# Performance work log

Measured on AMD Instinct MI355X. Metric: run time of the kernel, lower is better.

The kernel has to match this reference:

```python
import jax, jax.numpy as jnp
import numpy as np

B, S, D, DFF, H, V, L = 2, 1024, 1024, 4096, 16, 32000, 8
DH = D // H
EPS = 1e-5

def _pe():
    pos = np.arange(S, dtype=np.float32)[:, None]
    div = np.exp(np.arange(0, D, 2, dtype=np.float32) * (-np.log(10000.0) / D))
    pe = np.zeros((S, D), dtype=np.float32)
    pe[:, 0::2] = np.sin(pos * div)
    pe[:, 1::2] = np.cos(pos * div)
    return jnp.asarray(pe)

PE = _pe()

def _ln(h, g, b):
    m = jnp.mean(h, axis=-1, keepdims=True)
    v = jnp.mean((h - m) ** 2, axis=-1, keepdims=True)
    return (h - m) * jax.lax.rsqrt(v + EPS) * g + b

def setup_inputs():
    key = jax.random.key(0)
    k = jax.random.split(key, 16)
    sc = 0.02
    return {
        'x': jax.random.randint(k[0], (B, S), 0, V),
        'mask': jnp.tril(jnp.ones((1, 1, S, S), dtype=bool)),
        'emb': jax.random.normal(k[1], (V, D)) * sc,
        'Wq': jax.random.normal(k[2], (L, D, D)) * sc,
        'Wk': jax.random.normal(k[3], (L, D, D)) * sc,
        'Wv': jax.random.normal(k[4], (L, D, D)) * sc,
        'Wo': jax.random.normal(k[5], (L, D, D)) * sc,
        'ln1_g': jnp.ones((L, D)), 'ln1_b': jnp.zeros((L, D)),
        'ln2_g': jnp.ones((L, D)), 'ln2_b': jnp.zeros((L, D)),
        'W1': jax.random.normal(k[6], (L, D, DFF)) * sc,
        'b1': jnp.zeros((L, DFF)),
        'W2': jax.random.normal(k[7], (L, DFF, D)) * sc,
        'b2': jnp.zeros((L, D)),
        'lnf_g': jnp.ones((D,)), 'lnf_b': jnp.zeros((D,)),
        'projW': jax.random.normal(k[8], (D, V)) * sc,
        'projb': jnp.zeros((V,)),
    }

def reference(x, mask, emb, Wq, Wk, Wv, Wo, ln1_g, ln1_b, ln2_g, ln2_b,
              W1, b1, W2, b2, lnf_g, lnf_b, projW, projb):
    # embedding * sqrt(D) + positional encoding
    h = emb[x] * jnp.sqrt(jnp.float32(D)) + PE[None, :, :]
    scale = 1.0 / jnp.sqrt(jnp.float32(DH))
    for i in range(L):
        # --- self-attention sublayer (pre-LN residual) ---
        a_in = _ln(h, ln1_g[i], ln1_b[i])
        q = (a_in @ Wq[i]).reshape(B, S, H, DH)
        kk = (a_in @ Wk[i]).reshape(B, S, H, DH)
        v = (a_in @ Wv[i]).reshape(B, S, H, DH)
        scores = jnp.einsum('bqhd,bkhd->bhqk', q, kk) * scale
        scores = jnp.where(mask, scores, -1e9)
        attn = jax.nn.softmax(scores, axis=-1)
        o = jnp.einsum('bhqk,bkhd->bqhd', attn, v).reshape(B, S, D)
        h = h + o @ Wo[i]
        # --- feed-forward sublayer ---
        f_in = _ln(h, ln2_g[i], ln2_b[i])
        h = h + (jax.nn.relu(f_in @ W1[i] + b1[i]) @ W2[i] + b2[i])
    h = _ln(h, lnf_g, lnf_b)
    return h @ projW + projb
```

## Files before the change

### kernel.cpp

```cpp
#include <hip/hip_runtime.h>

typedef __bf16 bf16;
typedef __bf16 bf16x4 __attribute__((ext_vector_type(4)));
typedef __bf16 bf16x8 __attribute__((ext_vector_type(8)));
typedef float f32x4 __attribute__((ext_vector_type(4)));
typedef short short4v __attribute__((ext_vector_type(4)));

__device__ __forceinline__ short f2bs(float x) {
  bf16 hv = (bf16)x;
  return __builtin_bit_cast(short, hv);
}

__device__ __forceinline__ void gl_lds16(const void* g, void* l) {
  __builtin_amdgcn_global_load_lds(
      (const __attribute__((address_space(1))) unsigned int*)g,
      (__attribute__((address_space(3))) unsigned int*)l, 16, 0, 0);
}

__global__ __launch_bounds__(256) void wt_k(const float* __restrict__ in,
    bf16* __restrict__ out, int K, int N, long in_ls, long out_ls)
{
  __shared__ float t[64][33];
  const int z = blockIdx.z;
  const float* ip = in + (size_t)z * in_ls;
  bf16* op = out + (size_t)z * out_ls;
  const int n0 = blockIdx.x * 32, k0 = blockIdx.y * 64;
  const int tid = threadIdx.x;
  const int kr = tid >> 3, nc = (tid & 7) * 4;
#pragma unroll
  for (int hh = 0; hh < 2; ++hh) {
    float4 v = *(const float4*)(ip + (size_t)(k0 + kr + hh * 32) * N + n0 + nc);
    t[kr + hh * 32][nc]     = v.x;
    t[kr + hh * 32][nc + 1] = v.y;
    t[kr + hh * 32][nc + 2] = v.z;
    t[kr + hh * 32][nc + 3] = v.w;
  }
  __syncthreads();
  const int nr = tid >> 3, kc = (tid & 7) * 8;
  bf16x8 o;
#pragma unroll
  for (int j = 0; j < 8; ++j) o[j] = (bf16)t[kc + j][nr];
  *(bf16x8*)(op + (size_t)(n0 + nr) * K + k0 + kc) = o;
}

__global__ __launch_bounds__(256) void embed_k(const int* __restrict__ x,
    const float* __restrict__ emb, float* __restrict__ h)
{
  const int m = blockIdx.x, t = threadIdx.x;
  const int s = m & 1023;
  const int tok = x[m];
  const int d0 = t * 4;
  float4 e = *(const float4*)(emb + (size_t)tok * 1024 + d0);
  const float* ep = &e.x;
  float r[4];
#pragma unroll
  for (int j = 0; j < 4; ++j) {
    int d = d0 + j;
    float freq = expf((float)(d & ~1) * (-9.2103403719761836f / 1024.f));
    float ang = (float)s * freq;
    float pe = (d & 1) ? cosf(ang) : sinf(ang);
    r[j] = ep[j] * 32.f + pe;
  }
  *(float4*)(h + (size_t)m * 1024 + d0) = make_float4(r[0], r[1], r[2], r[3]);
}

__global__ __launch_bounds__(256) void ln_k(const float* __restrict__ h,
    const float* __restrict__ g, const float* __restrict__ b,
    bf16* __restrict__ out)
{
  const int row = blockIdx.x, t = threadIdx.x;
  const float* hr = h + (size_t)row * 1024;
  float4 x = *(const float4*)(hr + t * 4);
  float s  = x.x + x.y + x.z + x.w;
  float ss = x.x * x.x + x.y * x.y + x.z * x.z + x.w * x.w;
#pragma unroll
  for (int off = 32; off >= 1; off >>= 1) {
    s  += __shfl_down(s, off);
    ss += __shfl_down(ss, off);
  }
  __shared__ float sb[4], ssb[4];
  if ((t & 63) == 0) { sb[t >> 6] = s; ssb[t >> 6] = ss; }
  __syncthreads();
  s  = sb[0] + sb[1] + sb[2] + sb[3];
  ss = ssb[0] + ssb[1] + ssb[2] + ssb[3];
  const float mean = s * (1.f / 1024.f);
  const float var  = ss * (1.f / 1024.f) - mean * mean;
  const float rstd = rsqrtf(var + 1e-5f);
  const float* xp = &x.x;
#pragma unroll
  for (int j = 0; j < 4; ++j) {
    int d = t * 4 + j;
    out[(size_t)row * 1024 + d] = (bf16)((xp[j] - mean) * rstd * g[d] + b[d]);
  }
}

template<int MODE, int NSPLIT>
__global__ __launch_bounds__(256) void gemm3_k(
    const bf16* __restrict__ A, const bf16* __restrict__ Bt,
    const float* __restrict__ bias, void* __restrict__ Cout,
    float* __restrict__ Hacc, bf16* __restrict__ Vt,
    int M, int N, int K)
{
  __shared__ __align__(16) bf16 As[2][128 * 64];
  __shared__ __align__(16) bf16 Bs[2][128 * 64];

  const int nwg = gridDim.x;
  const int orig = blockIdx.x;
  const int q8 = nwg >> 3, r8 = nwg & 7;
  const int xcd = orig & 7, loc = orig >> 3;
  const int wg = (xcd < r8 ? xcd * (q8 + 1) : r8 * (q8 + 1) + (xcd - r8) * q8) + loc;
  const int nrowt = M >> 7;
  const int ntiles = nrowt * (N >> 7);
  const int split = (NSPLIT > 1) ? (wg / ntiles) : 0;
  const int tile  = (NSPLIT > 1) ? (wg % ntiles) : wg;
  const int rowt = tile & (nrowt - 1);
  const int colt = tile / nrowt;
  const int m0 = rowt * 128;
  const int n0 = colt * 128;
  const int Ks = K / NSPLIT;
  const int k_begin = split * Ks;
  const int nt = Ks >> 6;

  const int tid = threadIdx.x;
  const int lane = tid & 63;
  const int wbase = tid & ~63;
  const int wid = tid >> 6;
  const int wm = wid >> 1, wn = wid & 1;
  const int qr = lane & 15, grp = lane >> 4;

  f32x4 acc[4][4];
#pragma unroll
  for (int i = 0; i < 4; ++i)
#pragma unroll
    for (int j = 0; j < 4; ++j) acc[i][j] = (f32x4){0.f, 0.f, 0.f, 0.f};

  auto stage = [&](int bufi, int kt) {
#pragma unroll
    for (int it = 0; it < 4; ++it) {
      const int idx = it * 256 + tid;
      const int row = idx >> 3, c = idx & 7;
      const int bo = (c * 16) ^ ((row & 7) << 4);
      gl_lds16((const char*)(A + (size_t)(m0 + row) * K + kt) + bo,
               (char*)&As[bufi][0] + (size_t)(it * 256 + wbase) * 16);
    }
#pragma unroll
    for (int it = 0; it < 4; ++it) {
      const int idx = it * 256 + tid;
      const int row = idx >> 3, c = idx & 7;
      const int bo = (c * 16) ^ ((row & 7) << 4);
      gl_lds16((const char*)(Bt + (size_t)(n0 + row) * K + kt) + bo,
               (char*)&Bs[bufi][0] + (size_t)(it * 256 + wbase) * 16);
    }
  };

  stage(0, k_begin);
  asm volatile("s_waitcnt vmcnt(0)" ::: "memory");
  __builtin_amdgcn_s_barrier();

  for (int t = 0; t < nt; ++t) {
    const int cur = t & 1;
    if (t + 1 < nt) stage(cur ^ 1, k_begin + (t + 1) * 64);
#pragma unroll
    for (int ks = 0; ks < 2; ++ks) {
      bf16x8 af[4], bfr[4];
#pragma unroll
      for (int mi = 0; mi < 4; ++mi) {
        const int arow = wm * 64 + mi * 16 + qr;
        const int ab = arow * 128 + ((grp * 16 + ks * 64) ^ ((arow & 7) << 4));
        af[mi] = *(const bf16x8*)((const char*)&As[cur][0] + ab);
      }
#pragma unroll
      for (int ni = 0; ni < 4; ++ni) {
        const int brow = wn * 64 + ni * 16 + qr;
        const int bb = brow * 128 + ((grp * 16 + ks * 64) ^ ((brow & 7) << 4));
        bfr[ni] = *(const bf16x8*)((const char*)&Bs[cur][0] + bb);
      }
#pragma unroll
      for (int mi = 0; mi < 4; ++mi)
#pragma unroll
        for (int ni = 0; ni < 4; ++ni)
          acc[mi][ni] = __builtin_amdgcn_mfma_f32_16x16x32_bf16(
              af[mi], bfr[ni], acc[mi][ni], 0, 0, 0);
    }
    asm volatile("s_waitcnt vmcnt(0)" ::: "memory");
    __builtin_amdgcn_s_barrier();
  }

  const int sel = (MODE == 5) ? (n0 >> 10) : 0;
#pragma unroll
  for (int ni = 0; ni < 4; ++ni) {
    const int coln = wn * 64 + ni * 16 + qr;
    const int colg = n0 + coln;
    float bv = 0.f;
    if (MODE == 1 || MODE == 4) bv = bias[colg];
    if (MODE == 3 && split == 0) bv = bias[colg];
#pragma unroll
    for (int mi = 0; mi < 4; ++mi) {
      const int rowg0 = m0 + wm * 64 + mi * 16 + grp * 4;
      if (MODE == 5 && sel == 2) {
        const int b = rowg0 >> 10, s = rowg0 & 1023;
        bf16x4 pv;
#pragma unroll
        for (int r = 0; r < 4; ++r) pv[r] = (bf16)acc[mi][ni][r];
        *(bf16x4*)(Vt + (size_t)b * 1024 * 1024 + (size_t)(colg & 1023) * 1024 + s) = pv;
      } else {
#pragma unroll
        for (int r = 0; r < 4; ++r) {
          const int rowg = rowg0 + r;
          float v = acc[mi][ni][r];
          if (MODE == 1) {
            v += bv; v = v > 0.f ? v : 0.f;
            ((bf16*)Cout)[(size_t)rowg * N + colg] = (bf16)v;
          } else if (MODE == 2) {
            if (NSPLIT > 1) atomicAdd(&Hacc[(size_t)rowg * N + colg], v);
            else            Hacc[(size_t)rowg * N + colg] += v;
          } else if (MODE == 3) {
            if (NSPLIT > 1) atomicAdd(&Hacc[(size_t)rowg * N + colg], v + bv);
            else            Hacc[(size_t)rowg * N + colg] += v + bv;
          } else if (MODE == 4) {
            ((float*)Cout)[(size_t)rowg * N + colg] = v + bv;
          } else {
            bf16* cb = (bf16*)Cout + (size_t)sel * 2048 * 1024;
            cb[(size_t)rowg * 1024 + (colg & 1023)] = (bf16)v;
          }
        }
      }
    }
  }
}

__global__ __launch_bounds__(64) void attn_k(const bf16* __restrict__ qm,
    const bf16* __restrict__ km, const bf16* __restrict__ vt,
    bf16* __restrict__ om)
{
  const int lane = threadIdx.x;
  const int qr = lane & 15, g = lane >> 4;
  const int qt = blockIdx.x & 63;
  const int hh = (blockIdx.x >> 6) & 15;
  const int bb = blockIdx.x >> 10;
  const size_t rowb = (size_t)bb * 1024;
  const int hb = hh * 64;

  const bf16* qp = qm + (rowb + qt * 16 + qr) * 1024 + hb + g * 8;
  const bf16x8 qf0 = *(const bf16x8*)qp;
  const bf16x8 qf1 = *(const bf16x8*)(qp + 32);

  float m_run = -1e30f, l_run = 0.f;
  f32x4 oacc[4];
#pragma unroll
  for (int dt = 0; dt < 4; ++dt) oacc[dt] = (f32x4){0.f, 0.f, 0.f, 0.f};

  const int qglob = qt * 16 + qr;
  const bf16* vtb = vt + (size_t)bb * 1024 * 1024;

  for (int kvt = 0; kvt <= qt; ++kvt) {
    const bf16* kp = km + (rowb + kvt * 16 + qr) * 1024 + hb + g * 8;
    bf16x8 kf0 = *(const bf16x8*)kp;
    bf16x8 kf1 = *(const bf16x8*)(kp + 32);
    f32x4 st = (f32x4){0.f, 0.f, 0.f, 0.f};
    st = __builtin_amdgcn_mfma_f32_16x16x32_bf16(kf0, qf0, st, 0, 0, 0);
    st = __builtin_amdgcn_mfma_f32_16x16x32_bf16(kf1, qf1, st, 0, 0, 0);

    float sc[4];
#pragma unroll
    for (int r = 0; r < 4; ++r) {
      int kvg = kvt * 16 + g * 4 + r;
      sc[r] = (kvg <= qglob) ? st[r] * 0.125f : -1e30f;
    }
    float mloc = fmaxf(fmaxf(sc[0], sc[1]), fmaxf(sc[2], sc[3]));
    mloc = fmaxf(mloc, __shfl_xor(mloc, 16));
    mloc = fmaxf(mloc, __shfl_xor(mloc, 32));
    float m_new = fmaxf(m_run, mloc);
    float alpha = __expf(m_run - m_new);
    float p[4], ps = 0.f;
#pragma unroll
    for (int r = 0; r < 4; ++r) { p[r] = __expf(sc[r] - m_new); ps += p[r]; }
    ps += __shfl_xor(ps, 16);
    ps += __shfl_xor(ps, 32);
    l_run = l_run * alpha + ps;
    m_run = m_new;

    short4v pf;
#pragma unroll
    for (int r = 0; r < 4; ++r) pf[r] = f2bs(p[r]);
#pragma unroll
    for (int dt = 0; dt < 4; ++dt) oacc[dt] *= alpha;

#pragma unroll
    for (int dt = 0; dt < 4; ++dt) {
      short4v vf = __builtin_bit_cast(short4v,
          *(const bf16x4*)(vtb + (size_t)(hb + dt * 16 + qr) * 1024 + kvt * 16 + g * 4));
      oacc[dt] = __builtin_amdgcn_mfma_f32_16x16x16bf16_1k(vf, pf, oacc[dt], 0, 0, 0);
    }
  }

  const float inv = 1.f / l_run;
  bf16* op = om + (rowb + qt * 16 + qr) * 1024 + hb;
#pragma unroll
  for (int dt = 0; dt < 4; ++dt)
#pragma unroll
    for (int r = 0; r < 4; ++r)
      op[dt * 16 + g * 4 + r] = (bf16)(oacc[dt][r] * inv);
}

extern "C" void kernel_launch(void* const* d_in, const int* in_sizes, int n_in,
                              void* d_out, int out_size, void* d_ws, size_t ws_size,
                              hipStream_t stream)
{
  (void)in_sizes; (void)n_in; (void)out_size; (void)ws_size;
  const int*   x     = (const int*)d_in[0];
  const float* emb   = (const float*)d_in[2];
  const float* Wq    = (const float*)d_in[3];
  const float* Wk    = (const float*)d_in[4];
  const float* Wv    = (const float*)d_in[5];
  const float* Wo    = (const float*)d_in[6];
  const float* ln1g  = (const float*)d_in[7];
  const float* ln1b  = (const float*)d_in[8];
  const float* ln2g  = (const float*)d_in[9];
  const float* ln2b  = (const float*)d_in[10];
  const float* W1    = (const float*)d_in[11];
  const float* b1    = (const float*)d_in[12];
  const float* W2    = (const float*)d_in[13];
  const float* b2    = (const float*)d_in[14];
  const float* lnfg  = (const float*)d_in[15];
  const float* lnfb  = (const float*)d_in[16];
  const float* projW = (const float*)d_in[17];
  const float* projb = (const float*)d_in[18];

  char* ws = (char*)d_ws;
  const size_t MB = 1u << 20;
  float* h    = (float*)(ws + 0);
  bf16*  ain  = (bf16*)(ws + 8 * MB);
  bf16*  qb   = (bf16*)(ws + 12 * MB);
  bf16*  kb   = (bf16*)(ws + 16 * MB);
  bf16*  vtb  = (bf16*)(ws + 20 * MB);
  bf16*  ob   = (bf16*)(ws + 24 * MB);
  bf16*  mid  = (bf16*)(ws + 28 * MB);
  bf16*  Bqkv = (bf16*)(ws + 44 * MB);
  bf16*  Bo   = (bf16*)(ws + 92 * MB);
  bf16*  B1t  = (bf16*)(ws + 108 * MB);
  bf16*  B2t  = (bf16*)(ws + 172 * MB);
  bf16*  Bprj = (bf16*)(ws + 236 * MB);

  const long M1 = 1024 * 1024, M3 = 3 * M1, M4 = 4 * M1;

  wt_k<<<dim3(32, 16, 8),   256, 0, stream>>>(Wq, Bqkv,          1024, 1024, M1, M3);
  wt_k<<<dim3(32, 16, 8),   256, 0, stream>>>(Wk, Bqkv + M1,     1024, 1024, M1, M3);
  wt_k<<<dim3(32, 16, 8),   256, 0, stream>>>(Wv, Bqkv + 2 * M1, 1024, 1024, M1, M3);
  wt_k<<<dim3(32, 16, 8),   256, 0, stream>>>(Wo, Bo,            1024, 1024, M1, M1);
  wt_k<<<dim3(128, 16, 8),  256, 0, stream>>>(W1, B1t,           1024, 4096, M4, M4);
  wt_k<<<dim3(32, 64, 8),   256, 0, stream>>>(W2, B2t,           4096, 1024, M4, M4);
  wt_k<<<dim3(1000, 16, 1), 256, 0, stream>>>(projW, Bprj,       1024, 32000, 0, 0);

  embed_k<<<dim3(2048), 256, 0, stream>>>(x, emb, h);
  for (int i = 0; i < 8; ++i) {
    ln_k<<<dim3(2048), 256, 0, stream>>>(h, ln1g + i * 1024, ln1b + i * 1024, ain);
    gemm3_k<5,1><<<dim3(384), 256, 0, stream>>>(ain, Bqkv + i * M3, nullptr,
                                                qb, nullptr, vtb, 2048, 3072, 1024);
    attn_k<<<dim3(2048), 64, 0, stream>>>(qb, kb, vtb, ob);
    gemm3_k<2,2><<<dim3(256), 256, 0, stream>>>(ob, Bo + i * M1, nullptr,
                                                nullptr, h, nullptr, 2048, 1024, 1024);
    ln_k<<<dim3(2048), 256, 0, stream>>>(h, ln2g + i * 1024, ln2b + i * 1024, ain);
    gemm3_k<1,1><<<dim3(512), 256, 0, stream>>>(ain, B1t + i * M4, b1 + i * 4096,
                                                mid, nullptr, nullptr, 2048, 4096, 1024);
    gemm3_k<3,2><<<dim3(256), 256, 0, stream>>>(mid, B2t + i * M4, b2 + i * 1024,
                                                nullptr, h, nullptr, 2048, 1024, 4096);
  }
  ln_k<<<dim3(2048), 256, 0, stream>>>(h, lnfg, lnfb, ain);
  gemm3_k<4,1><<<dim3(4000), 256, 0, stream>>>(ain, Bprj, projb,
                                               d_out, nullptr, nullptr, 2048, 32000, 1024);
}
```

Baseline: 2.197 ms.

## Use 256x256-tile GEMM for vocab projection and unroll unmasked attention tiles

Adds a 512-thread GEMM kernel with 256x256 tiles, swizzled LDS double buffering and a staggered B prefetch, and uses it for the final 32000-wide output projection in place of the 128-tile generic GEMM. The goal is more operand reuse per loaded byte. The attention kernel now processes off-diagonal KV tiles two at a time without mask checks, and only the diagonal tile is masked, which cuts per-tile compare and shuffle overhead and gives more loads in flight. The larger tile uses much more LDS and registers, which may limit occupancy.

```diff
diff --git a/kernel.cpp b/kernel.cpp
--- a/kernel.cpp
+++ b/kernel.cpp
@@ -91,6 +91,111 @@
   for (int j = 0; j < 4; ++j) {
     int d = t * 4 + j;
     out[(size_t)row * 1024 + d] = (bf16)((xp[j] - mean) * rstd * g[d] + b[d]);
+  }
+}
+
+__global__ __launch_bounds__(512, 2) void gemm256_k(
+    const bf16* __restrict__ A, const bf16* __restrict__ Bt,
+    const float* __restrict__ bias, float* __restrict__ C,
+    int M, int N, int K)
+{
+  __shared__ __align__(16) bf16 As[2][256 * 64];
+  __shared__ __align__(16) bf16 Bs[2][256 * 64];
+
+  const int nwg = gridDim.x;
+  const int orig = blockIdx.x;
+  const int q8 = nwg >> 3, r8 = nwg & 7;
+  const int xcd = orig & 7, loc = orig >> 3;
+  const int wg = (xcd < r8 ? xcd * (q8 + 1) : r8 * (q8 + 1) + (xcd - r8) * q8) + loc;
+  const int nrowt = M >> 8;
+  const int rowt = wg & (nrowt - 1);
+  const int colt = wg / nrowt;
+  const int m0 = rowt * 256;
+  const int n0 = colt * 256;
+  const int nt = K >> 6;
+
+  const int tid = threadIdx.x;
+  const int lane = tid & 63;
+  const int wbase = tid & ~63;
+  const int wid = tid >> 6;
+  const int wm = wid >> 2, wn = wid & 3;
+  const int qr = lane & 15, grp = lane >> 4;
+
+  f32x4 acc[8][4];
+#pragma unroll
+  for (int i = 0; i < 8; ++i)
+#pragma unroll
+    for (int j = 0; j < 4; ++j) acc[i][j] = (f32x4){0.f, 0.f, 0.f, 0.f};
+
+  auto stageA = [&](int bufi, int kt) {
+#pragma unroll
+    for (int it = 0; it < 4; ++it) {
+      const int idx = it * 512 + tid;
+      const int row = idx >> 3, c = idx & 7;
+      const int bo = (c * 16) ^ ((row & 7) << 4);
+      gl_lds16((const char*)(A + (size_t)(m0 + row) * K + kt) + bo,
+               (char*)&As[bufi][0] + (size_t)(it * 512 + wbase) * 16);
+    }
+  };
+  auto stageB = [&](int bufi, int kt) {
+#pragma unroll
+    for (int it = 0; it < 4; ++it) {
+      const int idx = it * 512 + tid;
+      const int row = idx >> 3, c = idx & 7;
+      const int bo = (c * 16) ^ ((row & 7) << 4);
+      gl_lds16((const char*)(Bt + (size_t)(n0 + row) * K + kt) + bo,
+               (char*)&Bs[bufi][0] + (size_t)(it * 512 + wbase) * 16);
+    }
+  };
+
+  stageA(0, 0); stageB(0, 0);
+  asm volatile("s_waitcnt vmcnt(0)" ::: "memory");
+  __builtin_amdgcn_s_barrier();
+
+  for (int t = 0; t < nt; ++t) {
+    const int cur = t & 1;
+    const bool pfch = (t + 1 < nt);
+    if (pfch) stageA(cur ^ 1, (t + 1) * 64);
+#pragma unroll
+    for (int ks = 0; ks < 2; ++ks) {
+      bf16x8 af[8], bfr[4];
+#pragma unroll
+      for (int mi = 0; mi < 8; ++mi) {
+        const int arow = wm * 128 + mi * 16 + qr;
+        const int ab = arow * 128 + ((grp * 16 + ks * 64) ^ ((arow & 7) << 4));
+        af[mi] = *(const bf16x8*)((const char*)&As[cur][0] + ab);
+      }
+#pragma unroll
+      for (int ni = 0; ni < 4; ++ni) {
+        const int brow = wn * 64 + ni * 16 + qr;
+        const int bb = brow * 128 + ((grp * 16 + ks * 64) ^ ((brow & 7) << 4));
+        bfr[ni] = *(const bf16x8*)((const char*)&Bs[cur][0] + bb);
+      }
+      __builtin_amdgcn_s_setprio(1);
+#pragma unroll
+      for (int mi = 0; mi < 8; ++mi)
+#pragma unroll
+        for (int ni = 0; ni < 4; ++ni)
+          acc[mi][ni] = __builtin_amdgcn_mfma_f32_16x16x32_bf16(
+              af[mi], bfr[ni], acc[mi][ni], 0, 0, 0);
+      __builtin_amdgcn_s_setprio(0);
+      if (ks == 0 && pfch) stageB(cur ^ 1, (t + 1) * 64);
+    }
+    asm volatile("s_waitcnt vmcnt(0)" ::: "memory");
+    __builtin_amdgcn_s_barrier();
+  }
+
+#pragma unroll
+  for (int ni = 0; ni < 4; ++ni) {
+    const int colg = n0 + wn * 64 + ni * 16 + qr;
+    const float bv = bias[colg];
+#pragma unroll
+    for (int mi = 0; mi < 8; ++mi) {
+      const int rowg0 = m0 + wm * 128 + mi * 16 + grp * 4;
+#pragma unroll
+      for (int r = 0; r < 4; ++r)
+        C[(size_t)(rowg0 + r) * N + colg] = acc[mi][ni][r] + bv;
+    }
   }
 }
 
@@ -192,7 +297,7 @@
     const int coln = wn * 64 + ni * 16 + qr;
     const int colg = n0 + coln;
     float bv = 0.f;
-    if (MODE == 1 || MODE == 4) bv = bias[colg];
+    if (MODE == 1) bv = bias[colg];
     if (MODE == 3 && split == 0) bv = bias[colg];
 #pragma unroll
     for (int mi = 0; mi < 4; ++mi) {
@@ -217,9 +322,7 @@
           } else if (MODE == 3) {
             if (NSPLIT > 1) atomicAdd(&Hacc[(size_t)rowg * N + colg], v + bv);
             else            Hacc[(size_t)rowg * N + colg] += v + bv;
-          } else if (MODE == 4) {
-            ((float*)Cout)[(size_t)rowg * N + colg] = v + bv;
-          } else {
+          } else if (MODE == 5) {
             bf16* cb = (bf16*)Cout + (size_t)sel * 2048 * 1024;
             cb[(size_t)rowg * 1024 + (colg & 1023)] = (bf16)v;
           }
@@ -252,20 +355,24 @@
 
   const int qglob = qt * 16 + qr;
   const bf16* vtb = vt + (size_t)bb * 1024 * 1024;
-
-  for (int kvt = 0; kvt <= qt; ++kvt) {
-    const bf16* kp = km + (rowb + kvt * 16 + qr) * 1024 + hb + g * 8;
+  const bf16* kbase = km + rowb * 1024 + hb;
+
+  auto tile_step = [&](int kvt, bool masked) {
+    const bf16* kp = kbase + (size_t)kvt * 16 * 1024 + qr * 1024 + g * 8;
     bf16x8 kf0 = *(const bf16x8*)kp;
     bf16x8 kf1 = *(const bf16x8*)(kp + 32);
+    bf16x4 vf[4];
+#pragma unroll
+    for (int dt = 0; dt < 4; ++dt)
+      vf[dt] = *(const bf16x4*)(vtb + (size_t)(hb + dt * 16 + qr) * 1024 + kvt * 16 + g * 4);
     f32x4 st = (f32x4){0.f, 0.f, 0.f, 0.f};
     st = __builtin_amdgcn_mfma_f32_16x16x32_bf16(kf0, qf0, st, 0, 0, 0);
     st = __builtin_amdgcn_mfma_f32_16x16x32_bf16(kf1, qf1, st, 0, 0, 0);
-
     float sc[4];
 #pragma unroll
     for (int r = 0; r < 4; ++r) {
-      int kvg = kvt * 16 + g * 4 + r;
-      sc[r] = (kvg <= qglob) ? st[r] * 0.125f : -1e30f;
+      sc[r] = st[r] * 0.125f;
+      if (masked && (kvt * 16 + g * 4 + r > qglob)) sc[r] = -1e30f;
     }
     float mloc = fmaxf(fmaxf(sc[0], sc[1]), fmaxf(sc[2], sc[3]));
     mloc = fmaxf(mloc, __shfl_xor(mloc, 16));
@@ -279,20 +386,74 @@
     ps += __shfl_xor(ps, 32);
     l_run = l_run * alpha + ps;
     m_run = m_new;
-
-    short4v pf;
-#pragma unroll
-    for (int r = 0; r < 4; ++r) pf[r] = f2bs(p[r]);
-#pragma unroll
-    for (int dt = 0; dt < 4; ++dt) oacc[dt] *= alpha;
-
+    short4v pfa;
+#pragma unroll
+    for (int r = 0; r < 4; ++r) pfa[r] = f2bs(p[r]);
 #pragma unroll
     for (int dt = 0; dt < 4; ++dt) {
-      short4v vf = __builtin_bit_cast(short4v,
-          *(const bf16x4*)(vtb + (size_t)(hb + dt * 16 + qr) * 1024 + kvt * 16 + g * 4));
-      oacc[dt] = __builtin_amdgcn_mfma_f32_16x16x16bf16_1k(vf, pf, oacc[dt], 0, 0, 0);
-    }
-  }
+      oacc[dt] *= alpha;
+      oacc[dt] = __builtin_amdgcn_mfma_f32_16x16x16bf16_1k(
+          __builtin_bit_cast(short4v, vf[dt]), pfa, oacc[dt], 0, 0, 0);
+    }
+  };
+
+  const int nun = qt;
+  int kvt = 0;
+  for (; kvt + 1 < nun; kvt += 2) {
+    const bf16* kpa = kbase + (size_t)kvt * 16 * 1024 + qr * 1024 + g * 8;
+    const bf16* kpb = kpa + 16 * 1024;
+    bf16x8 ka0 = *(const bf16x8*)kpa;
+    bf16x8 ka1 = *(const bf16x8*)(kpa + 32);
+    bf16x8 kb0 = *(const bf16x8*)kpb;
+    bf16x8 kb1 = *(const bf16x8*)(kpb + 32);
+    bf16x4 vfa[4], vfb[4];
+#pragma unroll
+    for (int dt = 0; dt < 4; ++dt) {
+      const bf16* vp = vtb + (size_t)(hb + dt * 16 + qr) * 1024 + kvt * 16 + g * 4;
+      vfa[dt] = *(const bf16x4*)vp;
+      vfb[dt] = *(const bf16x4*)(vp + 16);
+    }
+    f32x4 sa = (f32x4){0.f, 0.f, 0.f, 0.f};
+    f32x4 sb = (f32x4){0.f, 0.f, 0.f, 0.f};
+    sa = __builtin_amdgcn_mfma_f32_16x16x32_bf16(ka0, qf0, sa, 0, 0, 0);
+    sb = __builtin_amdgcn_mfma_f32_16x16x32_bf16(kb0, qf0, sb, 0, 0, 0);
+    sa = __builtin_amdgcn_mfma_f32_16x16x32_bf16(ka1, qf1, sa, 0, 0, 0);
+    sb = __builtin_amdgcn_mfma_f32_16x16x32_bf16(kb1, qf1, sb, 0, 0, 0);
+    float pa[4], pb[4];
+    float mloc = -1e30f;
+#pragma unroll
+    for (int r = 0; r < 4; ++r) {
+      pa[r] = sa[r] * 0.125f; pb[r] = sb[r] * 0.125f;
+      mloc = fmaxf(mloc, fmaxf(pa[r], pb[r]));
+    }
+    mloc = fmaxf(mloc, __shfl_xor(mloc, 16));
+    mloc = fmaxf(mloc, __shfl_xor(mloc, 32));
+    float m_new = fmaxf(m_run, mloc);
+    float alpha = __expf(m_run - m_new);
+    float ps = 0.f;
+#pragma unroll
+    for (int r = 0; r < 4; ++r) {
+      pa[r] = __expf(pa[r] - m_new); pb[r] = __expf(pb[r] - m_new);
+      ps += pa[r] + pb[r];
+    }
+    ps += __shfl_xor(ps, 16);
+    ps += __shfl_xor(ps, 32);
+    l_run = l_run * alpha + ps;
+    m_run = m_new;
+    short4v pfa, pfb;
+#pragma unroll
+    for (int r = 0; r < 4; ++r) { pfa[r] = f2bs(pa[r]); pfb[r] = f2bs(pb[r]); }
+#pragma unroll
+    for (int dt = 0; dt < 4; ++dt) {
+      oacc[dt] *= alpha;
+      oacc[dt] = __builtin_amdgcn_mfma_f32_16x16x16bf16_1k(
+          __builtin_bit_cast(short4v, vfa[dt]), pfa, oacc[dt], 0, 0, 0);
+      oacc[dt] = __builtin_amdgcn_mfma_f32_16x16x16bf16_1k(
+          __builtin_bit_cast(short4v, vfb[dt]), pfb, oacc[dt], 0, 0, 0);
+    }
+  }
+  for (; kvt < nun; ++kvt) tile_step(kvt, false);
+  tile_step(qt, true);
 
   const float inv = 1.f / l_run;
   bf16* op = om + (rowb + qt * 16 + qr) * 1024 + hb;
@@ -367,6 +528,6 @@
                                                 nullptr, h, nullptr, 2048, 1024, 4096);
   }
   ln_k<<<dim3(2048), 256, 0, stream>>>(h, lnfg, lnfb, ain);
-  gemm3_k<4,1><<<dim3(4000), 256, 0, stream>>>(ain, Bprj, projb,
-                                               d_out, nullptr, nullptr, 2048, 32000, 1024);
-}
+  gemm256_k<<<dim3(1000), 512, 0, stream>>>(ain, Bprj, projb,
+                                            (float*)d_out, 2048, 32000, 1024);
+}
```

Measured after the change: 2.170 ms. Within noise of the previous version (-1.3%).
